# Optimization experiments

Hardware: AMD Instinct MI355X
Metric: run time of the kernel (lower is better)

Reference implementation:

```python
import jax, jax.numpy as jnp
import numpy as np

NUM_HEADS = 16
KEY_SIZE = 128
D_MODEL = NUM_HEADS * KEY_SIZE  # 2048; model_size defaults to num_heads*key_size
B, S = 4, 4096
EPS = 1e-6
MASK_NEG = -1e9


def setup_inputs() -> dict:
    key = jax.random.key(0)
    ks = jax.random.split(key, 8)
    query = jax.random.normal(ks[0], (B, S, D_MODEL), dtype=jnp.float32)
    key_t = jax.random.normal(ks[1], (B, S, D_MODEL), dtype=jnp.float32)
    value = jax.random.normal(ks[2], (B, S, D_MODEL), dtype=jnp.float32)
    # mask broadcast-added to attn_logits of shape [B, S, H, H]; 1 = masked out
    mask = jax.random.randint(ks[3], (B, S, NUM_HEADS, NUM_HEADS), 0, 2).astype(jnp.float32)
    w_scale = 0.02
    Wq = jax.random.normal(ks[4], (D_MODEL, NUM_HEADS * KEY_SIZE), dtype=jnp.float32) * w_scale
    Wk = jax.random.normal(ks[5], (D_MODEL, NUM_HEADS * KEY_SIZE), dtype=jnp.float32) * w_scale
    Wv = jax.random.normal(ks[6], (D_MODEL, NUM_HEADS * KEY_SIZE), dtype=jnp.float32) * w_scale
    Wo = jax.random.normal(ks[7], (NUM_HEADS * KEY_SIZE, D_MODEL), dtype=jnp.float32) * w_scale
    return {"query": query, "key": key_t, "value": value, "mask": mask,
            "Wq": Wq, "Wk": Wk, "Wv": Wv, "Wo": Wo}


def _split_heads(x):
    # [B, S, H*D] -> [B, H, S, D]  (matches tf reshape + transpose(0,2,1,3))
    b, s, _ = x.shape
    return x.reshape(b, s, NUM_HEADS, KEY_SIZE).transpose(0, 2, 1, 3)


def reference(query, key, value, mask, Wq, Wk, Wv, Wo):
    qh = _split_heads(query @ Wq)   # [B, H, S, D]
    kh = _split_heads(key @ Wk)     # [B, H, S, D]
    vh = _split_heads(value @ Wv)   # [B, H, S, D]

    # sum_normalization=True
    qh = qh / (jnp.sum(qh, axis=-1, keepdims=True) + EPS)
    kh = kh / (jnp.sum(kh, axis=-1, keepdims=True) + EPS)

    # Literal tf einsum '...thd,...Thd->...htT' on [B,H,S,D] tensors:
    # t/T bind to the head axis, h binds to the sequence axis.
    # attn_logits: [B, S, H, H]
    attn_logits = jnp.einsum('bqsd,bksd->bsqk', qh, kh)
    attn_logits = attn_logits + mask * MASK_NEG

    # use_softmax=True
    attn_weights = jax.nn.softmax(attn_logits / np.sqrt(float(KEY_SIZE)), axis=-1)

    # Literal tf einsum '...htT,...Thd->...thd' -> [B, H, S, D]
    attn = jnp.einsum('bsqk,bksd->bqsd', attn_weights, vh)
    # _combine_heads: transpose(0,2,1,3) then reshape -> [B, S, H*D]
    attn = attn.transpose(0, 2, 1, 3).reshape(attn.shape[0], attn.shape[2], NUM_HEADS * KEY_SIZE)
    out = attn @ Wo
    return (out, attn_weights)
```

## Files before the change

### kernel.cpp

```cpp
#include <hip/hip_runtime.h>
#include <hip/hip_fp16.h>

#define NHEAD 16
#define DHEAD 128
#define DMODEL 2048
#define SEQ 4096
#define BATCH 4
#define MROWS (BATCH*SEQ)

typedef _Float16 f16x8 __attribute__((ext_vector_type(8)));
typedef _Float16 f16x4 __attribute__((ext_vector_type(4)));
typedef float f32x4 __attribute__((ext_vector_type(4)));

__device__ inline void split8(const float* __restrict__ x, _Float16* __restrict__ hi,
                              _Float16* __restrict__ lo, int i8) {
  float4 v0 = ((const float4*)x)[2 * i8];
  float4 v1 = ((const float4*)x)[2 * i8 + 1];
  f16x8 h, l;
  h[0] = (_Float16)v0.x; h[1] = (_Float16)v0.y;
  h[2] = (_Float16)v0.z; h[3] = (_Float16)v0.w;
  h[4] = (_Float16)v1.x; h[5] = (_Float16)v1.y;
  h[6] = (_Float16)v1.z; h[7] = (_Float16)v1.w;
  ((f16x8*)hi)[i8] = h;
  if (lo) {
    l[0] = (_Float16)(v0.x - (float)h[0]);
    l[1] = (_Float16)(v0.y - (float)h[1]);
    l[2] = (_Float16)(v0.z - (float)h[2]);
    l[3] = (_Float16)(v0.w - (float)h[3]);
    l[4] = (_Float16)(v1.x - (float)h[4]);
    l[5] = (_Float16)(v1.y - (float)h[5]);
    l[6] = (_Float16)(v1.z - (float)h[6]);
    l[7] = (_Float16)(v1.w - (float)h[7]);
    ((f16x8*)lo)[i8] = l;
  }
}

__global__ __launch_bounds__(256) void split_f32_f16(
    const float* __restrict__ x, _Float16* __restrict__ hi,
    _Float16* __restrict__ lo, int n8) {
  int i = blockIdx.x * blockDim.x + threadIdx.x;
  int stride = gridDim.x * blockDim.x;
  for (; i < n8; i += stride) split8(x, hi, lo, i);
}

__global__ __launch_bounds__(256) void split_all(
    const float* __restrict__ q, const float* __restrict__ k,
    const float* __restrict__ v,
    _Float16* __restrict__ qh, _Float16* __restrict__ ql,
    _Float16* __restrict__ kh, _Float16* __restrict__ kl,
    _Float16* __restrict__ vh, int n8) {
  const float* x; _Float16* hi; _Float16* lo;
  if (blockIdx.y == 0)      { x = q; hi = qh; lo = ql; }
  else if (blockIdx.y == 1) { x = k; hi = kh; lo = kl; }
  else                      { x = v; hi = vh; lo = nullptr; }
  int i = blockIdx.x * blockDim.x + threadIdx.x;
  int stride = gridDim.x * blockDim.x;
  for (; i < n8; i += stride) split8(x, hi, lo, i);
}

__device__ inline void transpose_body(const float* __restrict__ W,
                                      _Float16* __restrict__ hi,
                                      _Float16* __restrict__ lo,
                                      int bx, int by, int tx, int ty) {
  __shared__ float tile[32][33];
  int c = bx * 32 + tx;
  for (int r0 = 0; r0 < 32; r0 += 8) {
    int r = by * 32 + ty + r0;
    tile[ty + r0][tx] = W[(size_t)r * DMODEL + c];
  }
  __syncthreads();
  for (int r0 = 0; r0 < 32; r0 += 8) {
    int n = bx * 32 + ty + r0;
    int k = by * 32 + tx;
    float v = tile[tx][ty + r0];
    _Float16 h = (_Float16)v;
    hi[(size_t)n * DMODEL + k] = h;
    if (lo) lo[(size_t)n * DMODEL + k] = (_Float16)(v - (float)h);
  }
}

__global__ __launch_bounds__(256) void transpose_split(
    const float* __restrict__ W, _Float16* __restrict__ hi,
    _Float16* __restrict__ lo) {
  transpose_body(W, hi, lo, blockIdx.x, blockIdx.y, threadIdx.x, threadIdx.y);
}

__global__ __launch_bounds__(256) void transpose_all(
    const float* __restrict__ Wq, const float* __restrict__ Wk,
    const float* __restrict__ Wv, const float* __restrict__ Wo,
    _Float16* __restrict__ qh, _Float16* __restrict__ ql,
    _Float16* __restrict__ kh, _Float16* __restrict__ kl,
    _Float16* __restrict__ vh, _Float16* __restrict__ oh) {
  const float* W; _Float16* hi; _Float16* lo;
  switch (blockIdx.z) {
    case 0:  W = Wq; hi = qh; lo = ql;      break;
    case 1:  W = Wk; hi = kh; lo = kl;      break;
    case 2:  W = Wv; hi = vh; lo = nullptr; break;
    default: W = Wo; hi = oh; lo = nullptr; break;
  }
  transpose_body(W, hi, lo, blockIdx.x, blockIdx.y, threadIdx.x, threadIdx.y);
}

__global__ __launch_bounds__(256) void colsum_f64(
    const float* __restrict__ W, float* __restrict__ CS) {
  const int k = blockIdx.x;
  const int t = threadIdx.x;
  const int h = t >> 4, s = t & 15;
  double acc = 0.0;
  const float* p = W + (size_t)k * DMODEL + h * DHEAD + s * 8;
#pragma unroll
  for (int i = 0; i < 8; i++) acc += (double)p[i];
#pragma unroll
  for (int m = 1; m < 16; m <<= 1) acc += __shfl_xor(acc, m, 64);
  if (s == 0) CS[(size_t)h * DMODEL + k] = (float)acc;
}

__global__ __launch_bounds__(256) void rowsum_v3(
    const float* __restrict__ q, const float* __restrict__ k,
    const float* __restrict__ CSq, const float* __restrict__ CSk,
    float* __restrict__ rsQ, float* __restrict__ rsK) {
  const float* X;  const float* CS;  float* rs;
  if (blockIdx.y == 0) { X = q; CS = CSq; rs = rsQ; }
  else                 { X = k; CS = CSk; rs = rsK; }
  const int t = threadIdx.x;
  const int lane = t & 63, w = t >> 6;
  const int row0 = blockIdx.x * 8 + w * 2;

  const float4* x0 = (const float4*)(X + ((size_t)row0 << 11));
  const float4* x1 = (const float4*)(X + ((size_t)(row0 + 1) << 11));
  float4 xa[8], xb[8];
#pragma unroll
  for (int i = 0; i < 8; i++) {
    xa[i] = x0[i * 64 + lane];
    xb[i] = x1[i * 64 + lane];
  }
  const float4* cs4 = (const float4*)CS;

  for (int h = 0; h < 16; h++) {
    double a0 = 0.0, a1 = 0.0;
#pragma unroll
    for (int i = 0; i < 8; i++) {
      float4 cv = cs4[h * 512 + i * 64 + lane];
      a0 += (double)xa[i].x * (double)cv.x + (double)xa[i].y * (double)cv.y
          + (double)xa[i].z * (double)cv.z + (double)xa[i].w * (double)cv.w;
      a1 += (double)xb[i].x * (double)cv.x + (double)xb[i].y * (double)cv.y
          + (double)xb[i].z * (double)cv.z + (double)xb[i].w * (double)cv.w;
    }
#pragma unroll
    for (int m = 1; m < 64; m <<= 1) {
      a0 += __shfl_xor(a0, m, 64);
      a1 += __shfl_xor(a1, m, 64);
    }
    if (lane == 0) {
      rs[(size_t)row0 * NHEAD + h]       = (float)a0;
      rs[(size_t)(row0 + 1) * NHEAD + h] = (float)a1;
    }
  }
}

__device__ inline void glds16(const void* g, void* l) {
  __builtin_amdgcn_global_load_lds(
      (const __attribute__((address_space(1))) unsigned int*)g,
      (__attribute__((address_space(3))) unsigned int*)l, 16, 0, 0);
}

template <int NPASS, int OUT_HALF>
__global__ __launch_bounds__(256) void gemm_f16(
    const _Float16* __restrict__ Ahi, const _Float16* __restrict__ Alo,
    const _Float16* __restrict__ Bhi, const _Float16* __restrict__ Blo,
    float* __restrict__ Cf, _Float16* __restrict__ Ch,
    int M, int N, int Kd) {
  constexpr int TILE = 128 * 32;
  __shared__ _Float16 lds[(NPASS == 3 ? 4 : 2) * TILE];
  _Float16* sAh = lds;
  _Float16* sBh = lds + (NPASS == 3 ? 2 : 1) * TILE;
  _Float16* sAl = lds + TILE;
  _Float16* sBl = lds + 3 * TILE;

  const int t = threadIdx.x;
  const int lane = t & 63, wid = t >> 6;
  const int wm = wid >> 1, wn = wid & 1;
  const int lr = lane & 15, lk = (lane >> 4) * 8;

  const int mtiles = M >> 7, ntiles = N >> 7;
  const int nwg = mtiles * ntiles;
  const int qq = nwg >> 3;
  const int v = (blockIdx.x & 7) * qq + (blockIdx.x >> 3);
  const int mx = v / ntiles, ny = v % ntiles;
  const int m0 = mx * 128, n0 = ny * 128;

  f32x4 acc[4][4] = {};

  for (int k0 = 0; k0 < Kd; k0 += 32) {
#pragma unroll
    for (int i = 0; i < 2; i++) {
      int slot = t + i * 256;
      int row = slot >> 2, kc = (slot & 3) * 8;
      glds16(Ahi + (size_t)(m0 + row) * Kd + k0 + kc, sAh + slot * 8);
      glds16(Bhi + (size_t)(n0 + row) * Kd + k0 + kc, sBh + slot * 8);
      if (NPASS == 3) {
        glds16(Alo + (size_t)(m0 + row) * Kd + k0 + kc, sAl + slot * 8);
        glds16(Blo + (size_t)(n0 + row) * Kd + k0 + kc, sBl + slot * 8);
      }
    }
    __syncthreads();

    f16x8 ah[4], bh[4], al[4], bl[4];
#pragma unroll
    for (int f = 0; f < 4; f++) {
      ah[f] = *(const f16x8*)&sAh[(wm * 64 + f * 16 + lr) * 32 + lk];
      bh[f] = *(const f16x8*)&sBh[(wn * 64 + f * 16 + lr) * 32 + lk];
      if (NPASS == 3) {
        al[f] = *(const f16x8*)&sAl[(wm * 64 + f * 16 + lr) * 32 + lk];
        bl[f] = *(const f16x8*)&sBl[(wn * 64 + f * 16 + lr) * 32 + lk];
      }
    }
#pragma unroll
    for (int i = 0; i < 4; i++)
#pragma unroll
      for (int j = 0; j < 4; j++) {
        acc[i][j] = __builtin_amdgcn_mfma_f32_16x16x32_f16(ah[i], bh[j], acc[i][j], 0, 0, 0);
        if (NPASS == 3) {
          acc[i][j] = __builtin_amdgcn_mfma_f32_16x16x32_f16(ah[i], bl[j], acc[i][j], 0, 0, 0);
          acc[i][j] = __builtin_amdgcn_mfma_f32_16x16x32_f16(al[i], bh[j], acc[i][j], 0, 0, 0);
        }
      }
    __syncthreads();
  }

#pragma unroll
  for (int i = 0; i < 4; i++) {
    int row = m0 + wm * 64 + i * 16 + (lane >> 4) * 4;
#pragma unroll
    for (int j = 0; j < 4; j++) {
      int col = n0 + wn * 64 + j * 16 + (lane & 15);
#pragma unroll
      for (int r = 0; r < 4; r++) {
        if (OUT_HALF)
          Ch[(size_t)(row + r) * N + col] = (_Float16)acc[i][j][r];
        else
          Cf[(size_t)(row + r) * N + col] = acc[i][j][r];
      }
    }
  }
}

__global__ __launch_bounds__(256) void attn_kernel(
    const float* __restrict__ Q, const float* __restrict__ K,
    const _Float16* __restrict__ V, const float* __restrict__ mask,
    const float* __restrict__ rsQ, const float* __restrict__ rsK,
    float* __restrict__ wout, _Float16* __restrict__ aout) {
  __shared__ float lq[16][132], lkk[16][132], lv[16][132];
  __shared__ float lw[16][17];
  const int pos = blockIdx.x;
  const int t = threadIdx.x;
  const int h = t >> 4, j = t & 15;
  const size_t rowbase = (size_t)pos * DMODEL + h * DHEAD;

  const float iq = 1.f / (rsQ[(size_t)pos * NHEAD + h] + 1e-6f);
  const float ik = 1.f / (rsK[(size_t)pos * NHEAD + h] + 1e-6f);

  {
    const int dlo = 4 * j, dhi = 64 + 4 * j;
    float4 q0 = *(const float4*)&Q[rowbase + dlo];
    float4 q1 = *(const float4*)&Q[rowbase + dhi];
    q0.x *= iq; q0.y *= iq; q0.z *= iq; q0.w *= iq;
    q1.x *= iq; q1.y *= iq; q1.z *= iq; q1.w *= iq;
    *(float4*)&lq[h][dlo] = q0;
    *(float4*)&lq[h][dhi] = q1;
    float4 k0 = *(const float4*)&K[rowbase + dlo];
    float4 k1 = *(const float4*)&K[rowbase + dhi];
    k0.x *= ik; k0.y *= ik; k0.z *= ik; k0.w *= ik;
    k1.x *= ik; k1.y *= ik; k1.z *= ik; k1.w *= ik;
    *(float4*)&lkk[h][dlo] = k0;
    *(float4*)&lkk[h][dhi] = k1;
    f16x4 v0 = *(const f16x4*)&V[rowbase + dlo];
    f16x4 v1 = *(const f16x4*)&V[rowbase + dhi];
    float4 vf0 = {(float)v0[0], (float)v0[1], (float)v0[2], (float)v0[3]};
    float4 vf1 = {(float)v1[0], (float)v1[1], (float)v1[2], (float)v1[3]};
    *(float4*)&lv[h][dlo] = vf0;
    *(float4*)&lv[h][dhi] = vf1;
  }
  __syncthreads();

  const float4* qr = (const float4*)&lq[h][0];
  const float4* kr = (const float4*)&lkk[j][0];
  float dot = 0.f;
#pragma unroll
  for (int d4 = 0; d4 < 32; d4++) {
    float4 a = qr[d4], b = kr[d4];
    dot = fmaf(a.x, b.x, dot); dot = fmaf(a.y, b.y, dot);
    dot = fmaf(a.z, b.z, dot); dot = fmaf(a.w, b.w, dot);
  }
  float mk = mask[(size_t)pos * 256 + t];
  float x = (dot - 1e9f * mk) * 0.08838834764831845f;
  float mx = x;
#pragma unroll
  for (int m = 1; m < 16; m <<= 1) mx = fmaxf(mx, __shfl_xor(mx, m, 64));
  float e = expf(x - mx);
  float den = e;
#pragma unroll
  for (int m = 1; m < 16; m <<= 1) den += __shfl_xor(den, m, 64);
  float w = e / den;
  wout[(size_t)pos * 256 + t] = w;
  lw[h][j] = w;
  __syncthreads();

  float wreg[16];
#pragma unroll
  for (int k2 = 0; k2 < 16; k2++) wreg[k2] = lw[h][k2];
  float4 a0 = {0.f, 0.f, 0.f, 0.f}, a1 = {0.f, 0.f, 0.f, 0.f};
  const int dlo = 4 * j, dhi = 64 + 4 * j;
#pragma unroll
  for (int k2 = 0; k2 < 16; k2++) {
    float4 v0 = *(const float4*)&lv[k2][dlo];
    float4 v1 = *(const float4*)&lv[k2][dhi];
    float wk = wreg[k2];
    a0.x = fmaf(wk, v0.x, a0.x); a0.y = fmaf(wk, v0.y, a0.y);
    a0.z = fmaf(wk, v0.z, a0.z); a0.w = fmaf(wk, v0.w, a0.w);
    a1.x = fmaf(wk, v1.x, a1.x); a1.y = fmaf(wk, v1.y, a1.y);
    a1.z = fmaf(wk, v1.z, a1.z); a1.w = fmaf(wk, v1.w, a1.w);
  }
  f16x4 o0, o1;
  o0[0] = (_Float16)a0.x; o0[1] = (_Float16)a0.y;
  o0[2] = (_Float16)a0.z; o0[3] = (_Float16)a0.w;
  o1[0] = (_Float16)a1.x; o1[1] = (_Float16)a1.y;
  o1[2] = (_Float16)a1.z; o1[3] = (_Float16)a1.w;
  *(f16x4*)&aout[rowbase + dlo] = o0;
  *(f16x4*)&aout[rowbase + dhi] = o1;
}

extern "C" void kernel_launch(void* const* d_in, const int* in_sizes, int n_in,
                              void* d_out, int out_size, void* d_ws, size_t ws_size,
                              hipStream_t stream) {
  const float* query = (const float*)d_in[0];
  const float* key   = (const float*)d_in[1];
  const float* value = (const float*)d_in[2];
  const float* mask  = (const float*)d_in[3];
  const float* Wq = (const float*)d_in[4];
  const float* Wk = (const float*)d_in[5];
  const float* Wv = (const float*)d_in[6];
  const float* Wo = (const float*)d_in[7];

  float* out  = (float*)d_out;
  float* wout = out + (size_t)MROWS * DMODEL;

  const size_t SZ_HALF = (size_t)MROWS * DMODEL * 2;
  const size_t SZ_F32  = (size_t)MROWS * DMODEL * 4;
  const size_t SZ_W    = (size_t)DMODEL * DMODEL * 2;
  const size_t SZ_CS   = (size_t)DMODEL * NHEAD * 4;
  const size_t SZ_RS   = (size_t)MROWS * NHEAD * 4;

  const int n8 = MROWS * DMODEL / 8;
  const int ggrid = (MROWS / 128) * (DMODEL / 128);
  dim3 tgrid4(DMODEL / 32, DMODEL / 32, 4);
  dim3 tgrid(DMODEL / 32, DMODEL / 32);
  dim3 tblk(32, 8);
  dim3 rsgrid(MROWS / 8, 2);
  float* Qbuf = out;

  const size_t NEED_A = 5 * SZ_HALF + SZ_F32 + 6 * SZ_W + 2 * SZ_CS + 2 * SZ_RS;
  const size_t NEED_B = 3 * SZ_HALF + SZ_F32 + 2 * SZ_W + 2 * SZ_CS + 2 * SZ_RS;
  char* ws = (char*)d_ws;

  if (ws_size >= NEED_A) {
    size_t off = 0;
    _Float16* qh = (_Float16*)(ws + off); off += SZ_HALF;
    _Float16* ql = (_Float16*)(ws + off); off += SZ_HALF;
    _Float16* kh = (_Float16*)(ws + off); off += SZ_HALF;
    _Float16* kl = (_Float16*)(ws + off); off += SZ_HALF;
    _Float16* vh = (_Float16*)(ws + off); off += SZ_HALF;
    float*  Kbuf = (float*)   (ws + off); off += SZ_F32;
    _Float16* wqh = (_Float16*)(ws + off); off += SZ_W;
    _Float16* wql = (_Float16*)(ws + off); off += SZ_W;
    _Float16* wkh = (_Float16*)(ws + off); off += SZ_W;
    _Float16* wkl = (_Float16*)(ws + off); off += SZ_W;
    _Float16* wvh = (_Float16*)(ws + off); off += SZ_W;
    _Float16* woh = (_Float16*)(ws + off); off += SZ_W;
    float* CSq = (float*)(ws + off); off += SZ_CS;
    float* CSk = (float*)(ws + off); off += SZ_CS;
    float* rsQ = (float*)(ws + off); off += SZ_RS;
    float* rsK = (float*)(ws + off); off += SZ_RS;
    _Float16* Vbuf   = qh;
    _Float16* attn16 = ql;

    colsum_f64<<<DMODEL, 256, 0, stream>>>(Wq, CSq);
    colsum_f64<<<DMODEL, 256, 0, stream>>>(Wk, CSk);
    rowsum_v3<<<rsgrid, 256, 0, stream>>>(query, key, CSq, CSk, rsQ, rsK);
    transpose_all<<<tgrid4, tblk, 0, stream>>>(Wq, Wk, Wv, Wo, wqh, wql, wkh, wkl, wvh, woh);
    split_all<<<dim3(4096, 3), 256, 0, stream>>>(query, key, value, qh, ql, kh, kl, vh, n8);
    gemm_f16<3, 0><<<ggrid, 256, 0, stream>>>(qh, ql, wqh, wql, Qbuf, nullptr, MROWS, DMODEL, DMODEL);
    gemm_f16<3, 0><<<ggrid, 256, 0, stream>>>(kh, kl, wkh, wkl, Kbuf, nullptr, MROWS, DMODEL, DMODEL);
    gemm_f16<1, 1><<<ggrid, 256, 0, stream>>>(vh, nullptr, wvh, nullptr, nullptr, Vbuf, MROWS, DMODEL, DMODEL);
    attn_kernel<<<MROWS, 256, 0, stream>>>(Qbuf, Kbuf, Vbuf, mask, rsQ, rsK, wout, attn16);
    gemm_f16<1, 0><<<ggrid, 256, 0, stream>>>(attn16, nullptr, woh, nullptr, out, nullptr, MROWS, DMODEL, DMODEL);
    return;
  }

  if (ws_size < NEED_B) return;

  _Float16* a_hi  = (_Float16*)ws;
  _Float16* a_lo  = (_Float16*)(ws + SZ_HALF);
  float*    Kbuf  = (float*)   (ws + 2 * SZ_HALF);
  _Float16* Vbuf  = (_Float16*)(ws + 2 * SZ_HALF + SZ_F32);
  _Float16* wT_hi = (_Float16*)(ws + 3 * SZ_HALF + SZ_F32);
  _Float16* wT_lo = (_Float16*)(ws + 3 * SZ_HALF + SZ_F32 + SZ_W);
  float*    CSq   = (float*)   (ws + 3 * SZ_HALF + SZ_F32 + 2 * SZ_W);
  float*    CSk   = (float*)   (ws + 3 * SZ_HALF + SZ_F32 + 2 * SZ_W + SZ_CS);
  float*    rsQ   = (float*)   (ws + 3 * SZ_HALF + SZ_F32 + 2 * SZ_W + 2 * SZ_CS);
  float*    rsK   = (float*)   (ws + 3 * SZ_HALF + SZ_F32 + 2 * SZ_W + 2 * SZ_CS + SZ_RS);
  _Float16* attn16 = a_hi;

  colsum_f64<<<DMODEL, 256, 0, stream>>>(Wq, CSq);
  colsum_f64<<<DMODEL, 256, 0, stream>>>(Wk, CSk);
  rowsum_v3<<<rsgrid, 256, 0, stream>>>(query, key, CSq, CSk, rsQ, rsK);

  split_f32_f16<<<4096, 256, 0, stream>>>(query, a_hi, a_lo, n8);
  transpose_split<<<tgrid, tblk, 0, stream>>>(Wq, wT_hi, wT_lo);
  gemm_f16<3, 0><<<ggrid, 256, 0, stream>>>(a_hi, a_lo, wT_hi, wT_lo, Qbuf, nullptr, MROWS, DMODEL, DMODEL);
  split_f32_f16<<<4096, 256, 0, stream>>>(key, a_hi, a_lo, n8);
  transpose_split<<<tgrid, tblk, 0, stream>>>(Wk, wT_hi, wT_lo);
  gemm_f16<3, 0><<<ggrid, 256, 0, stream>>>(a_hi, a_lo, wT_hi, wT_lo, Kbuf, nullptr, MROWS, DMODEL, DMODEL);
  split_f32_f16<<<4096, 256, 0, stream>>>(value, a_hi, nullptr, n8);
  transpose_split<<<tgrid, tblk, 0, stream>>>(Wv, wT_hi, nullptr);
  gemm_f16<1, 1><<<ggrid, 256, 0, stream>>>(a_hi, nullptr, wT_hi, nullptr, nullptr, Vbuf, MROWS, DMODEL, DMODEL);
  attn_kernel<<<MROWS, 256, 0, stream>>>(Qbuf, Kbuf, Vbuf, mask, rsQ, rsK, wout, attn16);
  transpose_split<<<tgrid, tblk, 0, stream>>>(Wo, wT_hi, nullptr);
  gemm_f16<1, 0><<<ggrid, 256, 0, stream>>>(attn16, nullptr, wT_hi, nullptr, out, nullptr, MROWS, DMODEL, DMODEL);
}
```

Baseline: 1.791 ms.

## Add 256x256 double-buffered MFMA GEMM with 512 threads for projection GEMMs

Adds a new GEMM kernel with 256x256 output tiles, 512 threads (8 waves) and double-buffered LDS staging through global_load_lds. It uses manual s_waitcnt/sched_barrier pipelining, setprio around the MFMA groups, and an XCD-aware block remap. All four projection GEMMs in the fast path use it. The larger tiles are meant to raise operand reuse and overlap global loads with MFMA work, at the cost of heavy LDS use (128KB for the 3-pass variant) and 128 accumulator registers per thread, which may limit occupancy or spill.

```diff
diff --git a/kernel.cpp b/kernel.cpp
--- a/kernel.cpp
+++ b/kernel.cpp
@@ -164,6 +164,156 @@
       (__attribute__((address_space(3))) unsigned int*)l, 16, 0, 0);
 }
 
+#define DP_LGKM_P() do { \
+  if constexpr (NPASS == 3) asm volatile("s_waitcnt lgkmcnt(4)" ::: "memory"); \
+  else                      asm volatile("s_waitcnt lgkmcnt(2)" ::: "memory"); \
+  __builtin_amdgcn_sched_barrier(0); } while (0)
+#define DP_LGKM_0() do { \
+  asm volatile("s_waitcnt lgkmcnt(0)" ::: "memory"); \
+  __builtin_amdgcn_sched_barrier(0); } while (0)
+#define DP_VMCNT_P() do { \
+  if constexpr (NPASS == 3) asm volatile("s_waitcnt vmcnt(8)" ::: "memory"); \
+  else                      asm volatile("s_waitcnt vmcnt(4)" ::: "memory"); \
+  __builtin_amdgcn_sched_barrier(0); } while (0)
+#define DP_VMCNT_0() do { \
+  asm volatile("s_waitcnt vmcnt(0)" ::: "memory"); \
+  __builtin_amdgcn_sched_barrier(0); } while (0)
+#define DP_BAR() do { \
+  asm volatile("" ::: "memory"); \
+  __builtin_amdgcn_s_barrier(); \
+  asm volatile("" ::: "memory"); } while (0)
+#define DP_QUAD(AR, P) do { \
+  __builtin_amdgcn_s_setprio(1); \
+  _Pragma("unroll") \
+  for (int i_ = 0; i_ < 2; i_++) \
+    _Pragma("unroll") \
+    for (int n_ = 0; n_ < 4; n_++) { \
+      acc[2*(P)+i_][n_] = __builtin_amdgcn_mfma_f32_16x16x32_f16(AR[i_], bhF[n_], acc[2*(P)+i_][n_], 0, 0, 0); \
+      if constexpr (NPASS == 3) { \
+        acc[2*(P)+i_][n_] = __builtin_amdgcn_mfma_f32_16x16x32_f16(AR[i_], blF[n_], acc[2*(P)+i_][n_], 0, 0, 0); \
+        acc[2*(P)+i_][n_] = __builtin_amdgcn_mfma_f32_16x16x32_f16(AR[2+i_], bhF[n_], acc[2*(P)+i_][n_], 0, 0, 0); \
+      } \
+    } \
+  __builtin_amdgcn_s_setprio(0); } while (0)
+
+template <int NPASS, int OUT_HALF>
+__global__ __launch_bounds__(512, 2) void gemm_dp(
+    const _Float16* __restrict__ Ahi, const _Float16* __restrict__ Alo,
+    const _Float16* __restrict__ Bhi, const _Float16* __restrict__ Blo,
+    float* __restrict__ Cf, _Float16* __restrict__ Ch,
+    int M, int N, int Kd) {
+  extern __shared__ char smem_raw[];
+  constexpr int NMAT = (NPASS == 3) ? 4 : 2;
+  constexpr int BUFB = NMAT * 16384;
+  constexpr int BOFF = (NPASS == 3) ? 32768 : 16384;
+
+  const int t = threadIdx.x;
+  const int lane = t & 63, wid = t >> 6;
+  const int wm = wid >> 2, wn = wid & 3;
+  const int lr = lane & 15;
+  const int lkb = (lane >> 4) * 16;
+
+  const int mtiles = M >> 8, ntiles = N >> 8;
+  const int nwg = mtiles * ntiles;
+  const int qq = nwg >> 3;
+  const int v = (blockIdx.x & 7) * qq + (blockIdx.x >> 3);
+  const int m0 = (v / ntiles) << 8, n0 = (v % ntiles) << 8;
+  const int NT = Kd >> 5;
+
+  f32x4 acc[8][4] = {};
+  f16x8 bhF[4], blF[4], aA[4], aB[4];
+
+  auto STAGE = [&](int kt, int c) {
+    char* dstb = smem_raw + c * BUFB;
+    const size_t kOff = (size_t)kt << 5;
+#pragma unroll
+    for (int j = 0; j < NMAT * 2; j++) {
+      int s = t + j * 512;
+      int mm = s >> 10;
+      int r = (s & 1023) >> 2;
+      int c8 = (s & 3) << 3;
+      const _Float16* src; int rb;
+      if (mm == 0)      { src = Ahi; rb = m0 + r; }
+      else if (mm == 1) { src = (NPASS == 3) ? Alo : Bhi;
+                          rb = ((NPASS == 3) ? m0 : n0) + r; }
+      else if (mm == 2) { src = Bhi; rb = n0 + r; }
+      else              { src = Blo; rb = n0 + r; }
+      glds16(src + (size_t)rb * Kd + kOff + c8, dstb + (size_t)s * 16);
+    }
+  };
+  auto RD_B = [&](const char* buf) {
+#pragma unroll
+    for (int n = 0; n < 4; n++) {
+      int row = wn * 64 + n * 16 + lr;
+      bhF[n] = *(const f16x8*)(buf + BOFF + row * 64 + lkb);
+      if constexpr (NPASS == 3)
+        blF[n] = *(const f16x8*)(buf + BOFF + 16384 + row * 64 + lkb);
+    }
+  };
+  auto RD_A = [&](const char* buf, int p, f16x8* d) {
+#pragma unroll
+    for (int i = 0; i < 2; i++) {
+      int row = wm * 128 + (2 * p + i) * 16 + lr;
+      d[i] = *(const f16x8*)(buf + row * 64 + lkb);
+      if constexpr (NPASS == 3)
+        d[2 + i] = *(const f16x8*)(buf + 16384 + row * 64 + lkb);
+    }
+  };
+
+  STAGE(0, 0);
+  STAGE(1, 1);
+  DP_VMCNT_P();
+  DP_BAR();
+
+  for (int kt = 0; kt < NT; kt++) {
+    const char* buf = (const char*)smem_raw + (kt & 1) * BUFB;
+    RD_B(buf);
+    RD_A(buf, 0, aA);
+    RD_A(buf, 1, aB);
+    DP_LGKM_P();
+    DP_QUAD(aA, 0);
+    RD_A(buf, 2, aA);
+    DP_LGKM_P();
+    DP_QUAD(aB, 1);
+    RD_A(buf, 3, aB);
+    DP_LGKM_P();
+    DP_QUAD(aA, 2);
+    DP_LGKM_0();
+    DP_BAR();
+    if (kt + 2 < NT) {
+      STAGE(kt + 2, kt & 1);
+      DP_QUAD(aB, 3);
+      DP_VMCNT_P();
+    } else {
+      DP_QUAD(aB, 3);
+      DP_VMCNT_0();
+    }
+    DP_BAR();
+  }
+
+#pragma unroll
+  for (int mi = 0; mi < 8; mi++) {
+    int row = m0 + wm * 128 + mi * 16 + ((lane >> 4) << 2);
+#pragma unroll
+    for (int n = 0; n < 4; n++) {
+      int col = n0 + wn * 64 + n * 16 + (lane & 15);
+#pragma unroll
+      for (int r = 0; r < 4; r++) {
+        if constexpr (OUT_HALF)
+          Ch[(size_t)(row + r) * N + col] = (_Float16)acc[mi][n][r];
+        else
+          Cf[(size_t)(row + r) * N + col] = acc[mi][n][r];
+      }
+    }
+  }
+}
+#undef DP_LGKM_P
+#undef DP_LGKM_0
+#undef DP_VMCNT_P
+#undef DP_VMCNT_0
+#undef DP_BAR
+#undef DP_QUAD
+
 template <int NPASS, int OUT_HALF>
 __global__ __launch_bounds__(256) void gemm_f16(
     const _Float16* __restrict__ Ahi, const _Float16* __restrict__ Alo,
@@ -352,6 +502,7 @@
   const size_t SZ_RS   = (size_t)MROWS * NHEAD * 4;
 
   const int n8 = MROWS * DMODEL / 8;
+  const int dpgrid = (MROWS / 256) * (DMODEL / 256);
   const int ggrid = (MROWS / 128) * (DMODEL / 128);
   dim3 tgrid4(DMODEL / 32, DMODEL / 32, 4);
   dim3 tgrid(DMODEL / 32, DMODEL / 32);
@@ -389,11 +540,11 @@
     rowsum_v3<<<rsgrid, 256, 0, stream>>>(query, key, CSq, CSk, rsQ, rsK);
     transpose_all<<<tgrid4, tblk, 0, stream>>>(Wq, Wk, Wv, Wo, wqh, wql, wkh, wkl, wvh, woh);
     split_all<<<dim3(4096, 3), 256, 0, stream>>>(query, key, value, qh, ql, kh, kl, vh, n8);
-    gemm_f16<3, 0><<<ggrid, 256, 0, stream>>>(qh, ql, wqh, wql, Qbuf, nullptr, MROWS, DMODEL, DMODEL);
-    gemm_f16<3, 0><<<ggrid, 256, 0, stream>>>(kh, kl, wkh, wkl, Kbuf, nullptr, MROWS, DMODEL, DMODEL);
-    gemm_f16<1, 1><<<ggrid, 256, 0, stream>>>(vh, nullptr, wvh, nullptr, nullptr, Vbuf, MROWS, DMODEL, DMODEL);
+    gemm_dp<3, 0><<<dpgrid, 512, 131072, stream>>>(qh, ql, wqh, wql, Qbuf, nullptr, MROWS, DMODEL, DMODEL);
+    gemm_dp<3, 0><<<dpgrid, 512, 131072, stream>>>(kh, kl, wkh, wkl, Kbuf, nullptr, MROWS, DMODEL, DMODEL);
+    gemm_dp<1, 1><<<dpgrid, 512, 65536, stream>>>(vh, nullptr, wvh, nullptr, nullptr, Vbuf, MROWS, DMODEL, DMODEL);
     attn_kernel<<<MROWS, 256, 0, stream>>>(Qbuf, Kbuf, Vbuf, mask, rsQ, rsK, wout, attn16);
-    gemm_f16<1, 0><<<ggrid, 256, 0, stream>>>(attn16, nullptr, woh, nullptr, out, nullptr, MROWS, DMODEL, DMODEL);
+    gemm_dp<1, 0><<<dpgrid, 512, 65536, stream>>>(attn16, nullptr, woh, nullptr, out, nullptr, MROWS, DMODEL, DMODEL);
     return;
   }
 
```

Result: faster. 1.574 ms (-12.1%).

## Replace projection GEMMs with 256x256 double-buffered, software-pipelined MFMA kernel

Applied to the files above, without the earlier changes.

Adds a new gemm_dp kernel with 256x256 output tiles, 512 threads, and double-buffered LDS fed by global_load_lds. It uses XOR-swizzled LDS addressing, staggered lgkmcnt waits that interleave LDS reads with MFMAs, s_setprio around the MFMA bursts, and a block-index remap across XCD groups. All four projection GEMMs on the large-workspace path now use it. The aim is higher MFMA utilization and more data reuse per tile, in exchange for heavy register pressure, one block per CU, up to 128KB of dynamic LDS, and fragile hand-scheduled waits.

```diff
diff --git a/kernel.cpp b/kernel.cpp
--- a/kernel.cpp
+++ b/kernel.cpp
@@ -164,6 +164,164 @@
       (__attribute__((address_space(3))) unsigned int*)l, 16, 0, 0);
 }
 
+#define DP_WAIT(n_) do { \
+  asm volatile("s_waitcnt lgkmcnt(%0)" :: "n"(n_) : "memory"); \
+  __builtin_amdgcn_sched_barrier(0); } while (0)
+#define DP_SP(AR, H, P) do { \
+  __builtin_amdgcn_s_setprio(1); \
+  _Pragma("unroll") \
+  for (int i_ = 0; i_ < 2; i_++) \
+    _Pragma("unroll") \
+    for (int n_ = 0; n_ < 2; n_++) { \
+      acc[2*(P)+i_][2*(H)+n_] = __builtin_amdgcn_mfma_f32_16x16x32_f16(AR[i_], bh[H][n_], acc[2*(P)+i_][2*(H)+n_], 0, 0, 0); \
+      if constexpr (NPASS == 3) { \
+        acc[2*(P)+i_][2*(H)+n_] = __builtin_amdgcn_mfma_f32_16x16x32_f16(AR[i_], bl[H][n_], acc[2*(P)+i_][2*(H)+n_], 0, 0, 0); \
+        acc[2*(P)+i_][2*(H)+n_] = __builtin_amdgcn_mfma_f32_16x16x32_f16(AR[2+i_], bh[H][n_], acc[2*(P)+i_][2*(H)+n_], 0, 0, 0); \
+      } \
+    } \
+  __builtin_amdgcn_s_setprio(0); } while (0)
+
+template <int NPASS, int OUT_HALF>
+__global__ __launch_bounds__(512, 1) void gemm_dp(
+    const _Float16* __restrict__ Ahi, const _Float16* __restrict__ Alo,
+    const _Float16* __restrict__ Bhi, const _Float16* __restrict__ Blo,
+    float* __restrict__ Cf, _Float16* __restrict__ Ch,
+    int M, int N, int Kd) {
+  extern __shared__ char smem_raw[];
+  constexpr int NMAT = (NPASS == 3) ? 4 : 2;
+  constexpr int NLD  = NMAT * 2;
+  constexpr int BUFB = NMAT * 16384;
+  constexpr int BOFF = (NPASS == 3) ? 32768 : 16384;
+  constexpr int U    = (NPASS == 3) ? 4 : 2;
+
+  const int t = threadIdx.x;
+  const int lane = t & 63, wid = t >> 6;
+  const int wm = wid >> 2, wn = wid & 3;
+  const int lr = lane & 15;
+  const int lkbs = (((lane >> 4) ^ ((lr >> 1) & 3)) << 4);
+
+  const int mtiles = M >> 8, ntiles = N >> 8;
+  const int nwg = mtiles * ntiles;
+  const int qq = nwg >> 3;
+  const int v = (blockIdx.x & 7) * qq + (blockIdx.x >> 3);
+  const int m0 = (v / ntiles) << 8, n0 = (v % ntiles) << 8;
+  const int NT = Kd >> 5;
+
+  f32x4 acc[8][4] = {};
+  f16x8 bh[2][2], bl[2][2], a0[4], a1[4], a2[4];
+
+  const int r0i = t >> 2;
+  const int gsx = (t & 3) ^ ((r0i >> 1) & 3);
+  const char* gA0 = (const char*)(Ahi + (size_t)(m0 + r0i) * Kd + gsx * 8);
+  const char* gB0 = (const char*)(Bhi + (size_t)(n0 + r0i) * Kd + gsx * 8);
+  const char* gA1 = nullptr; const char* gB1 = nullptr;
+  if constexpr (NPASS == 3) {
+    gA1 = (const char*)(Alo + (size_t)(m0 + r0i) * Kd + gsx * 8);
+    gB1 = (const char*)(Blo + (size_t)(n0 + r0i) * Kd + gsx * 8);
+  }
+  const size_t RSTEP = (size_t)128 * Kd * sizeof(_Float16);
+
+  auto STAGE = [&](int kt, int c) {
+    char* d = smem_raw + c * BUFB + (t << 4);
+    const size_t kb = (size_t)kt << 6;
+    glds16(gA0 + kb,         d);
+    glds16(gA0 + kb + RSTEP, d + 8192);
+    if constexpr (NPASS == 3) {
+      glds16(gA1 + kb,         d + 16384);
+      glds16(gA1 + kb + RSTEP, d + 24576);
+      glds16(gB0 + kb,         d + 32768);
+      glds16(gB0 + kb + RSTEP, d + 40960);
+      glds16(gB1 + kb,         d + 49152);
+      glds16(gB1 + kb + RSTEP, d + 57344);
+    } else {
+      glds16(gB0 + kb,         d + 16384);
+      glds16(gB0 + kb + RSTEP, d + 24576);
+    }
+  };
+  auto RD_BH = [&](const char* buf, int h) {
+#pragma unroll
+    for (int n = 0; n < 2; n++) {
+      int row = wn * 64 + (2 * h + n) * 16 + lr;
+      bh[h][n] = *(const f16x8*)(buf + BOFF + row * 64 + lkbs);
+      if constexpr (NPASS == 3)
+        bl[h][n] = *(const f16x8*)(buf + BOFF + 16384 + row * 64 + lkbs);
+    }
+  };
+  auto RD_A = [&](const char* buf, int p, f16x8 (&d)[4]) {
+#pragma unroll
+    for (int i = 0; i < 2; i++) {
+      int row = wm * 128 + (2 * p + i) * 16 + lr;
+      d[i] = *(const f16x8*)(buf + row * 64 + lkbs);
+      if constexpr (NPASS == 3)
+        d[2 + i] = *(const f16x8*)(buf + 16384 + row * 64 + lkbs);
+    }
+  };
+
+  auto TILE = [&](f16x8 (&x)[4], f16x8 (&y)[4], f16x8 (&z)[4],
+                  int kt, bool pf) {
+    const char* buf  = (const char*)smem_raw + (kt & 1) * BUFB;
+    const char* bufN = (const char*)smem_raw + ((kt + 1) & 1) * BUFB;
+    DP_WAIT(2 * U);
+    DP_SP(x, 0, 0);
+    RD_A(buf, 2, z);
+    DP_WAIT(2 * U);
+    DP_SP(x, 1, 0);
+    RD_A(buf, 3, x);
+    DP_WAIT(2 * U);
+    DP_SP(y, 0, 1);
+    DP_SP(y, 1, 1);
+    DP_WAIT(U);
+    DP_SP(z, 0, 2);
+    DP_SP(z, 1, 2);
+    DP_WAIT(0);
+    DP_SP(x, 0, 3);
+    asm volatile("s_waitcnt vmcnt(0)" ::: "memory");
+    __builtin_amdgcn_sched_barrier(0);
+    __builtin_amdgcn_s_barrier();
+    if (kt + 2 < NT) STAGE(kt + 2, kt & 1);
+    if (pf) { RD_BH(bufN, 0); RD_A(bufN, 0, y); }
+    DP_SP(x, 1, 3);
+    if (pf) { RD_BH(bufN, 1); RD_A(bufN, 1, z); }
+  };
+
+  STAGE(0, 0);
+  STAGE(1, 1);
+  asm volatile("s_waitcnt vmcnt(%0)" :: "n"(NLD) : "memory");
+  __builtin_amdgcn_sched_barrier(0);
+  __builtin_amdgcn_s_barrier();
+  {
+    const char* buf0 = (const char*)smem_raw;
+    RD_BH(buf0, 0); RD_A(buf0, 0, a0);
+    RD_BH(buf0, 1); RD_A(buf0, 1, a1);
+  }
+
+  int kt = 0;
+  for (int it = 0; it < NT / 3; it++) {
+    TILE(a0, a1, a2, kt, true); kt++;
+    TILE(a1, a2, a0, kt, true); kt++;
+    TILE(a2, a0, a1, kt, true); kt++;
+  }
+  TILE(a0, a1, a2, kt, false);
+
+#pragma unroll
+  for (int mi = 0; mi < 8; mi++) {
+    int row = m0 + wm * 128 + mi * 16 + ((lane >> 4) << 2);
+#pragma unroll
+    for (int n = 0; n < 4; n++) {
+      int col = n0 + wn * 64 + n * 16 + (lane & 15);
+#pragma unroll
+      for (int r = 0; r < 4; r++) {
+        if constexpr (OUT_HALF)
+          Ch[(size_t)(row + r) * N + col] = (_Float16)acc[mi][n][r];
+        else
+          Cf[(size_t)(row + r) * N + col] = acc[mi][n][r];
+      }
+    }
+  }
+}
+#undef DP_WAIT
+#undef DP_SP
+
 template <int NPASS, int OUT_HALF>
 __global__ __launch_bounds__(256) void gemm_f16(
     const _Float16* __restrict__ Ahi, const _Float16* __restrict__ Alo,
@@ -352,6 +510,7 @@
   const size_t SZ_RS   = (size_t)MROWS * NHEAD * 4;
 
   const int n8 = MROWS * DMODEL / 8;
+  const int dpgrid = (MROWS / 256) * (DMODEL / 256);
   const int ggrid = (MROWS / 128) * (DMODEL / 128);
   dim3 tgrid4(DMODEL / 32, DMODEL / 32, 4);
   dim3 tgrid(DMODEL / 32, DMODEL / 32);
@@ -389,11 +548,11 @@
     rowsum_v3<<<rsgrid, 256, 0, stream>>>(query, key, CSq, CSk, rsQ, rsK);
     transpose_all<<<tgrid4, tblk, 0, stream>>>(Wq, Wk, Wv, Wo, wqh, wql, wkh, wkl, wvh, woh);
     split_all<<<dim3(4096, 3), 256, 0, stream>>>(query, key, value, qh, ql, kh, kl, vh, n8);
-    gemm_f16<3, 0><<<ggrid, 256, 0, stream>>>(qh, ql, wqh, wql, Qbuf, nullptr, MROWS, DMODEL, DMODEL);
-    gemm_f16<3, 0><<<ggrid, 256, 0, stream>>>(kh, kl, wkh, wkl, Kbuf, nullptr, MROWS, DMODEL, DMODEL);
-    gemm_f16<1, 1><<<ggrid, 256, 0, stream>>>(vh, nullptr, wvh, nullptr, nullptr, Vbuf, MROWS, DMODEL, DMODEL);
+    gemm_dp<3, 0><<<dpgrid, 512, 131072, stream>>>(qh, ql, wqh, wql, Qbuf, nullptr, MROWS, DMODEL, DMODEL);
+    gemm_dp<3, 0><<<dpgrid, 512, 131072, stream>>>(kh, kl, wkh, wkl, Kbuf, nullptr, MROWS, DMODEL, DMODEL);
+    gemm_dp<1, 1><<<dpgrid, 512, 65536, stream>>>(vh, nullptr, wvh, nullptr, nullptr, Vbuf, MROWS, DMODEL, DMODEL);
     attn_kernel<<<MROWS, 256, 0, stream>>>(Qbuf, Kbuf, Vbuf, mask, rsQ, rsK, wout, attn16);
-    gemm_f16<1, 0><<<ggrid, 256, 0, stream>>>(attn16, nullptr, woh, nullptr, out, nullptr, MROWS, DMODEL, DMODEL);
+    gemm_dp<1, 0><<<dpgrid, 512, 65536, stream>>>(attn16, nullptr, woh, nullptr, out, nullptr, MROWS, DMODEL, DMODEL);
     return;
   }
 
```

Result: slower. 1.938 ms (+8.2%).
